# Optimization experiments

Hardware: AMD Instinct MI355X
Metric: run time of the kernel (lower is better)

## Reference

```python
import jax, jax.numpy as jnp
import numpy as np

SEQ, BZ, DIM = 2048, 16, 1024
NUM_LANG, DICT_LEN = 16, 32000


def setup_inputs() -> dict:
    key = jax.random.key(0)
    ks = jax.random.split(key, 6)
    x = jax.random.normal(ks[0], (SEQ, BZ, DIM), dtype=jnp.float32)
    # raw language ids live at the tail of the dictionary: dict_len-1-raw in [0, num_lang)
    raw = DICT_LEN - 1 - jax.random.randint(ks[1], (BZ,), 0, NUM_LANG)
    W_base = jax.random.normal(ks[2], (DIM, DIM), dtype=jnp.float32) * (DIM ** -0.5)
    b_base = jax.random.normal(ks[3], (DIM,), dtype=jnp.float32) * 0.02
    W = jax.random.uniform(ks[4], (NUM_LANG, DIM, DIM), dtype=jnp.float32) * (DIM ** -0.5)
    bias = jax.random.uniform(ks[5], (NUM_LANG, DIM), dtype=jnp.float32)
    return {"x": x, "lang_ids": raw, "W_base": W_base, "b_base": b_base,
            "W": W, "bias": bias, "dict_len": DICT_LEN, "num_lang": NUM_LANG}


def reference(x, lang_ids, W_base, b_base, W, bias, dict_len, num_lang):
    # Map raw ids to expert indices in [0, num_lang)
    ids = dict_len - 1 - lang_ids                      # [bz]
    # base_model (nn.Linear): h = x @ W_base.T + b_base
    h = jnp.einsum('sbd,ed->sbe', x, W_base) + b_base  # [seq, bz, dim]
    # The original pads each language group to max group size, runs a batched
    # einsum 'abcd,ade->abce' over languages, then scatters back with per-lang
    # bias. Mathematically each batch column j gets W[lang_j] applied:
    We = W[ids]                                        # [bz, dim, dim]
    out = jnp.einsum('sbd,bde->sbe', h, We) + bias[ids][None, :, :]
    return out
```

## Files before the change

kernel.cpp:

```cpp
#include <hip/hip_runtime.h>
#include <stdint.h>

typedef unsigned short u16;
typedef unsigned int u32;
typedef __bf16 bf16x8 __attribute__((ext_vector_type(8)));
typedef float f32x4 __attribute__((ext_vector_type(4)));

#define SEQ 2048
#define BZ 16
#define DIM 1024

__device__ __forceinline__ u16 f2bf(float f) {
    union { float f; u32 u; } a; a.f = f;
    u32 r = a.u + 0x7FFFu + ((a.u >> 16) & 1u);
    return (u16)(r >> 16);
}
__device__ __forceinline__ float bf2f(u16 u) {
    union { u32 u; float f; } a; a.u = ((u32)u) << 16;
    return a.f;
}
__device__ __forceinline__ void async16(const u16* g, u16* l) {
    __builtin_amdgcn_global_load_lds(
        (const __attribute__((address_space(1))) void*)g,
        (__attribute__((address_space(3))) void*)l, 16, 0, 0);
}

__global__ void convert_x(const float* __restrict__ x, u16* __restrict__ xb)
{
    int s = blockIdx.x;
    int t = threadIdx.x;
    const float4* src = (const float4*)(x + (size_t)s * BZ * DIM);
    #pragma unroll
    for (int j = 0; j < 16; j++) {
        int idx = j * 256 + t;
        float4 v = src[idx];
        int e = idx * 4;
        int b = e >> 10, d = e & 1023;
        u32 lo = f2bf(v.x) | ((u32)f2bf(v.y) << 16);
        u32 hi = f2bf(v.z) | ((u32)f2bf(v.w) << 16);
        *(uint2*)(xb + ((size_t)b * SEQ + s) * DIM + d) = make_uint2(lo, hi);
    }
}

__global__ void transpose_cvt(const float* __restrict__ W,
                              const float* __restrict__ W_base,
                              const int* __restrict__ lang_ids,
                              const int* __restrict__ dict_len,
                              u16* __restrict__ Wt,
                              u16* __restrict__ Wbt)
{
    int z = blockIdx.z;
    const float* S;
    u16* D;
    if (z < BZ) {
        int id = dict_len[0] - 1 - lang_ids[z];
        S = W + (size_t)id * DIM * DIM;
        D = Wbt + (size_t)z * DIM * DIM;
    } else {
        S = W_base;
        D = Wt;
    }
    __shared__ float tile[32][33];
    int tx = threadIdx.x, ty = threadIdx.y;
    int x0 = blockIdx.x * 32, y0 = blockIdx.y * 32;
    #pragma unroll
    for (int i = 0; i < 4; i++)
        tile[ty + 8 * i][tx] = S[(size_t)(y0 + ty + 8 * i) * DIM + x0 + tx];
    __syncthreads();
    #pragma unroll
    for (int i = 0; i < 4; i++)
        D[(size_t)(x0 + ty + 8 * i) * DIM + y0 + tx] = f2bf(tile[tx][ty + 8 * i]);
}

__global__ void bb_kernel(const u16* __restrict__ Wbt,
                          const float* __restrict__ b_base,
                          const float* __restrict__ bias,
                          const int* __restrict__ lang_ids,
                          const int* __restrict__ dict_len,
                          float* __restrict__ bb)
{
    int gw = blockIdx.x * 4 + (threadIdx.x >> 6);
    int b = gw >> 10;
    int f = gw & 1023;
    int lane = threadIdx.x & 63;
    const u16* row = Wbt + ((size_t)b * DIM + f) * DIM;
    float s = 0.f;
    #pragma unroll
    for (int i = 0; i < DIM / 64; i++)
        s += bf2f(row[lane + 64 * i]) * b_base[lane + 64 * i];
    #pragma unroll
    for (int off = 32; off; off >>= 1)
        s += __shfl_xor(s, off, 64);
    if (lane == 0) {
        int id = dict_len[0] - 1 - lang_ids[b];
        bb[b * DIM + f] = s + bias[(size_t)id * DIM + f];
    }
}

__global__ void gemm1_kernel(const u16* __restrict__ Wbt,
                             const u16* __restrict__ Wt,
                             u16* __restrict__ CT)
{
    int b = blockIdx.z;
    int f0 = blockIdx.y * 128;
    int d0 = blockIdx.x * 128;
    const u16* A = Wbt + (size_t)b * DIM * DIM;
    const u16* B = Wt;
    u16* C = CT + (size_t)b * DIM * DIM;

    __shared__ u16 As[128 * 32];
    __shared__ u16 Bs[128 * 32];

    int tid = threadIdx.x;
    int wave = tid >> 6, lane = tid & 63;
    int wm = (wave >> 1) * 64, wn = (wave & 1) * 64;
    int quad = lane >> 4, lr = lane & 15;

    int srow = wave * 32 + (lane >> 2);
    int scol = (lane & 3) * 8;
    const u16* ga0 = A + (size_t)(f0 + srow) * DIM + scol;
    const u16* ga1 = ga0 + (size_t)16 * DIM;
    const u16* gb0 = B + (size_t)(d0 + srow) * DIM + scol;
    const u16* gb1 = gb0 + (size_t)16 * DIM;
    u16* la0 = &As[(wave * 32) * 32];
    u16* la1 = &As[(wave * 32 + 16) * 32];
    u16* lb0 = &Bs[(wave * 32) * 32];
    u16* lb1 = &Bs[(wave * 32 + 16) * 32];

    f32x4 acc[4][4];
    #pragma unroll
    for (int i = 0; i < 4; i++)
        #pragma unroll
        for (int j = 0; j < 4; j++)
            #pragma unroll
            for (int e = 0; e < 4; e++) acc[i][j][e] = 0.f;

    for (int k0 = 0; k0 < DIM; k0 += 32) {
        async16(ga0, la0); async16(ga1, la1);
        async16(gb0, lb0); async16(gb1, lb1);
        ga0 += 32; ga1 += 32; gb0 += 32; gb1 += 32;
        __syncthreads();
        bf16x8 af[4], bfv[4];
        #pragma unroll
        for (int mt = 0; mt < 4; mt++)
            af[mt] = *(const bf16x8*)&As[(wm + mt * 16 + lr) * 32 + quad * 8];
        #pragma unroll
        for (int nt = 0; nt < 4; nt++)
            bfv[nt] = *(const bf16x8*)&Bs[(wn + nt * 16 + lr) * 32 + quad * 8];
        #pragma unroll
        for (int mt = 0; mt < 4; mt++)
            #pragma unroll
            for (int nt = 0; nt < 4; nt++)
                acc[mt][nt] = __builtin_amdgcn_mfma_f32_16x16x32_bf16(
                    af[mt], bfv[nt], acc[mt][nt], 0, 0, 0);
        __syncthreads();
    }
    #pragma unroll
    for (int mt = 0; mt < 4; mt++) {
        int fr = f0 + wm + mt * 16 + quad * 4;
        #pragma unroll
        for (int nt = 0; nt < 4; nt++) {
            int dc = d0 + wn + nt * 16 + lr;
            #pragma unroll
            for (int rr = 0; rr < 4; rr++)
                C[(size_t)(fr + rr) * DIM + dc] = f2bf(acc[mt][nt][rr]);
        }
    }
}

__global__ void gemm2_kernel(const u16* __restrict__ xb,
                             const u16* __restrict__ CT,
                             const float* __restrict__ bb,
                             float* __restrict__ out)
{
    int b = blockIdx.z;
    int s0 = blockIdx.y * 128;
    int f0 = blockIdx.x * 128;
    const u16* A = xb + (size_t)b * SEQ * DIM;
    const u16* Bm = CT + (size_t)b * DIM * DIM;

    __shared__ u16 As[128 * 32];
    __shared__ u16 Bs[128 * 32];

    int tid = threadIdx.x;
    int wave = tid >> 6, lane = tid & 63;
    int wm = (wave >> 1) * 64, wn = (wave & 1) * 64;
    int quad = lane >> 4, lr = lane & 15;

    int srow = wave * 32 + (lane >> 2);
    int scol = (lane & 3) * 8;
    const u16* ga0 = A + (size_t)(s0 + srow) * DIM + scol;
    const u16* ga1 = ga0 + (size_t)16 * DIM;
    const u16* gb0 = Bm + (size_t)(f0 + srow) * DIM + scol;
    const u16* gb1 = gb0 + (size_t)16 * DIM;
    u16* la0 = &As[(wave * 32) * 32];
    u16* la1 = &As[(wave * 32 + 16) * 32];
    u16* lb0 = &Bs[(wave * 32) * 32];
    u16* lb1 = &Bs[(wave * 32 + 16) * 32];

    f32x4 acc[4][4];
    #pragma unroll
    for (int i = 0; i < 4; i++)
        #pragma unroll
        for (int j = 0; j < 4; j++)
            #pragma unroll
            for (int e = 0; e < 4; e++) acc[i][j][e] = 0.f;

    for (int k0 = 0; k0 < DIM; k0 += 32) {
        async16(ga0, la0); async16(ga1, la1);
        async16(gb0, lb0); async16(gb1, lb1);
        ga0 += 32; ga1 += 32; gb0 += 32; gb1 += 32;
        __syncthreads();
        bf16x8 af[4], bfv[4];
        #pragma unroll
        for (int mt = 0; mt < 4; mt++)
            af[mt] = *(const bf16x8*)&As[(wm + mt * 16 + lr) * 32 + quad * 8];
        #pragma unroll
        for (int nt = 0; nt < 4; nt++)
            bfv[nt] = *(const bf16x8*)&Bs[(wn + nt * 16 + lr) * 32 + quad * 8];
        #pragma unroll
        for (int mt = 0; mt < 4; mt++)
            #pragma unroll
            for (int nt = 0; nt < 4; nt++)
                acc[mt][nt] = __builtin_amdgcn_mfma_f32_16x16x32_bf16(
                    af[mt], bfv[nt], acc[mt][nt], 0, 0, 0);
        __syncthreads();
    }
    #pragma unroll
    for (int nt = 0; nt < 4; nt++) {
        int fcol = f0 + wn + nt * 16 + lr;
        float bv = bb[b * DIM + fcol];
        #pragma unroll
        for (int mt = 0; mt < 4; mt++) {
            int sr = s0 + wm + mt * 16 + quad * 4;
            #pragma unroll
            for (int rr = 0; rr < 4; rr++)
                out[((size_t)(sr + rr) * BZ + b) * DIM + fcol] = acc[mt][nt][rr] + bv;
        }
    }
}

extern "C" void kernel_launch(void* const* d_in, const int* in_sizes, int n_in,
                              void* d_out, int out_size, void* d_ws, size_t ws_size,
                              hipStream_t stream)
{
    const float* x        = (const float*)d_in[0];
    const int*   lang_ids = (const int*)d_in[1];
    const float* W_base   = (const float*)d_in[2];
    const float* b_base   = (const float*)d_in[3];
    const float* W        = (const float*)d_in[4];
    const float* bias     = (const float*)d_in[5];
    const int*   dict_len = (const int*)d_in[6];
    float* out = (float*)d_out;

    char* ws = (char*)d_ws;
    u16*  Wt  = (u16*)ws;
    u16*  Wbt = (u16*)(ws + (size_t)(2u << 20));
    u16*  CT  = (u16*)(ws + (size_t)(34u << 20));
    float* bb = (float*)(ws + (size_t)(66u << 20));
    u16*  xb  = (u16*)(ws + (size_t)(67u << 20));

    convert_x<<<dim3(SEQ, 1, 1), 256, 0, stream>>>(x, xb);
    transpose_cvt<<<dim3(32, 32, 17), dim3(32, 8, 1), 0, stream>>>(
        W, W_base, lang_ids, dict_len, Wt, Wbt);
    bb_kernel<<<dim3(4096, 1, 1), 256, 0, stream>>>(
        Wbt, b_base, bias, lang_ids, dict_len, bb);
    gemm1_kernel<<<dim3(8, 8, 16), 256, 0, stream>>>(Wbt, Wt, CT);
    gemm2_kernel<<<dim3(8, 16, 16), 256, 0, stream>>>(xb, CT, bb, out);
}
```

Measured before the change: 454.9 us.

## Double-buffer LDS tiles and remap GEMM blocks across XCDs

Both GEMM kernels now keep two LDS buffers and issue async global-to-LDS loads for the next K-slice while the current slice feeds MFMA, so load latency overlaps with compute. The 3D grid is flattened to 1D and remapped so that consecutive block IDs, which the hardware spreads round-robin over XCDs, land on the same batch and tile neighbourhood, aiming to improve L2 reuse per XCD. LDS use per block doubles, which may lower occupancy. The loop still relies on the trailing __syncthreads to make the prefetched data visible.

```diff
diff --git a/kernel.cpp b/kernel.cpp
--- a/kernel.cpp
+++ b/kernel.cpp
@@ -101,15 +101,19 @@
                              const u16* __restrict__ Wt,
                              u16* __restrict__ CT)
 {
-    int b = blockIdx.z;
-    int f0 = blockIdx.y * 128;
-    int d0 = blockIdx.x * 128;
+    int bid = blockIdx.x;
+    int virt = ((bid & 7) << 7) + (bid >> 3);
+    int b    = virt >> 6;
+    int rem  = virt & 63;
+    int f0   = (rem >> 3) << 7;
+    int d0   = (rem & 7) << 7;
+
     const u16* A = Wbt + (size_t)b * DIM * DIM;
     const u16* B = Wt;
     u16* C = CT + (size_t)b * DIM * DIM;
 
-    __shared__ u16 As[128 * 32];
-    __shared__ u16 Bs[128 * 32];
+    __shared__ u16 As[2 * 128 * 32];
+    __shared__ u16 Bs[2 * 128 * 32];
 
     int tid = threadIdx.x;
     int wave = tid >> 6, lane = tid & 63;
@@ -122,10 +126,7 @@
     const u16* ga1 = ga0 + (size_t)16 * DIM;
     const u16* gb0 = B + (size_t)(d0 + srow) * DIM + scol;
     const u16* gb1 = gb0 + (size_t)16 * DIM;
-    u16* la0 = &As[(wave * 32) * 32];
-    u16* la1 = &As[(wave * 32 + 16) * 32];
-    u16* lb0 = &Bs[(wave * 32) * 32];
-    u16* lb1 = &Bs[(wave * 32 + 16) * 32];
+    int lofs = wave * 32 * 32;
 
     f32x4 acc[4][4];
     #pragma unroll
@@ -135,18 +136,30 @@
             #pragma unroll
             for (int e = 0; e < 4; e++) acc[i][j][e] = 0.f;
 
+    async16(ga0, As + lofs); async16(ga1, As + lofs + 16 * 32);
+    async16(gb0, Bs + lofs); async16(gb1, Bs + lofs + 16 * 32);
+    ga0 += 32; ga1 += 32; gb0 += 32; gb1 += 32;
+    __syncthreads();
+
+    int cur = 0;
     for (int k0 = 0; k0 < DIM; k0 += 32) {
-        async16(ga0, la0); async16(ga1, la1);
-        async16(gb0, lb0); async16(gb1, lb1);
-        ga0 += 32; ga1 += 32; gb0 += 32; gb1 += 32;
-        __syncthreads();
+        int nxt = cur ^ 1;
+        if (k0 + 32 < DIM) {
+            u16* da = As + nxt * 4096 + lofs;
+            u16* db = Bs + nxt * 4096 + lofs;
+            async16(ga0, da); async16(ga1, da + 16 * 32);
+            async16(gb0, db); async16(gb1, db + 16 * 32);
+            ga0 += 32; ga1 += 32; gb0 += 32; gb1 += 32;
+        }
+        const u16* ra = As + cur * 4096;
+        const u16* rb = Bs + cur * 4096;
         bf16x8 af[4], bfv[4];
         #pragma unroll
         for (int mt = 0; mt < 4; mt++)
-            af[mt] = *(const bf16x8*)&As[(wm + mt * 16 + lr) * 32 + quad * 8];
+            af[mt] = *(const bf16x8*)&ra[(wm + mt * 16 + lr) * 32 + quad * 8];
         #pragma unroll
         for (int nt = 0; nt < 4; nt++)
-            bfv[nt] = *(const bf16x8*)&Bs[(wn + nt * 16 + lr) * 32 + quad * 8];
+            bfv[nt] = *(const bf16x8*)&rb[(wn + nt * 16 + lr) * 32 + quad * 8];
         #pragma unroll
         for (int mt = 0; mt < 4; mt++)
             #pragma unroll
@@ -154,6 +167,7 @@
                 acc[mt][nt] = __builtin_amdgcn_mfma_f32_16x16x32_bf16(
                     af[mt], bfv[nt], acc[mt][nt], 0, 0, 0);
         __syncthreads();
+        cur = nxt;
     }
     #pragma unroll
     for (int mt = 0; mt < 4; mt++) {
@@ -173,14 +187,18 @@
                              const float* __restrict__ bb,
                              float* __restrict__ out)
 {
-    int b = blockIdx.z;
-    int s0 = blockIdx.y * 128;
-    int f0 = blockIdx.x * 128;
-    const u16* A = xb + (size_t)b * SEQ * DIM;
+    int bid = blockIdx.x;
+    int virt = ((bid & 7) << 8) + (bid >> 3);
+    int b    = virt >> 7;
+    int rem  = virt & 127;
+    int s0   = (rem >> 3) << 7;
+    int f0   = (rem & 7) << 7;
+
+    const u16* A  = xb + (size_t)b * SEQ * DIM;
     const u16* Bm = CT + (size_t)b * DIM * DIM;
 
-    __shared__ u16 As[128 * 32];
-    __shared__ u16 Bs[128 * 32];
+    __shared__ u16 As[2 * 128 * 32];
+    __shared__ u16 Bs[2 * 128 * 32];
 
     int tid = threadIdx.x;
     int wave = tid >> 6, lane = tid & 63;
@@ -193,10 +211,7 @@
     const u16* ga1 = ga0 + (size_t)16 * DIM;
     const u16* gb0 = Bm + (size_t)(f0 + srow) * DIM + scol;
     const u16* gb1 = gb0 + (size_t)16 * DIM;
-    u16* la0 = &As[(wave * 32) * 32];
-    u16* la1 = &As[(wave * 32 + 16) * 32];
-    u16* lb0 = &Bs[(wave * 32) * 32];
-    u16* lb1 = &Bs[(wave * 32 + 16) * 32];
+    int lofs = wave * 32 * 32;
 
     f32x4 acc[4][4];
     #pragma unroll
@@ -206,18 +221,30 @@
             #pragma unroll
             for (int e = 0; e < 4; e++) acc[i][j][e] = 0.f;
 
+    async16(ga0, As + lofs); async16(ga1, As + lofs + 16 * 32);
+    async16(gb0, Bs + lofs); async16(gb1, Bs + lofs + 16 * 32);
+    ga0 += 32; ga1 += 32; gb0 += 32; gb1 += 32;
+    __syncthreads();
+
+    int cur = 0;
     for (int k0 = 0; k0 < DIM; k0 += 32) {
-        async16(ga0, la0); async16(ga1, la1);
-        async16(gb0, lb0); async16(gb1, lb1);
-        ga0 += 32; ga1 += 32; gb0 += 32; gb1 += 32;
-        __syncthreads();
+        int nxt = cur ^ 1;
+        if (k0 + 32 < DIM) {
+            u16* da = As + nxt * 4096 + lofs;
+            u16* db = Bs + nxt * 4096 + lofs;
+            async16(ga0, da); async16(ga1, da + 16 * 32);
+            async16(gb0, db); async16(gb1, db + 16 * 32);
+            ga0 += 32; ga1 += 32; gb0 += 32; gb1 += 32;
+        }
+        const u16* ra = As + cur * 4096;
+        const u16* rb = Bs + cur * 4096;
         bf16x8 af[4], bfv[4];
         #pragma unroll
         for (int mt = 0; mt < 4; mt++)
-            af[mt] = *(const bf16x8*)&As[(wm + mt * 16 + lr) * 32 + quad * 8];
+            af[mt] = *(const bf16x8*)&ra[(wm + mt * 16 + lr) * 32 + quad * 8];
         #pragma unroll
         for (int nt = 0; nt < 4; nt++)
-            bfv[nt] = *(const bf16x8*)&Bs[(wn + nt * 16 + lr) * 32 + quad * 8];
+            bfv[nt] = *(const bf16x8*)&rb[(wn + nt * 16 + lr) * 32 + quad * 8];
         #pragma unroll
         for (int mt = 0; mt < 4; mt++)
             #pragma unroll
@@ -225,6 +252,7 @@
                 acc[mt][nt] = __builtin_amdgcn_mfma_f32_16x16x32_bf16(
                     af[mt], bfv[nt], acc[mt][nt], 0, 0, 0);
         __syncthreads();
+        cur = nxt;
     }
     #pragma unroll
     for (int nt = 0; nt < 4; nt++) {
@@ -265,6 +293,6 @@
         W, W_base, lang_ids, dict_len, Wt, Wbt);
     bb_kernel<<<dim3(4096, 1, 1), 256, 0, stream>>>(
         Wbt, b_base, bias, lang_ids, dict_len, bb);
-    gemm1_kernel<<<dim3(8, 8, 16), 256, 0, stream>>>(Wbt, Wt, CT);
-    gemm2_kernel<<<dim3(8, 16, 16), 256, 0, stream>>>(xb, CT, bb, out);
-}
+    gemm1_kernel<<<dim3(1024, 1, 1), 256, 0, stream>>>(Wbt, Wt, CT);
+    gemm2_kernel<<<dim3(2048, 1, 1), 256, 0, stream>>>(xb, CT, bb, out);
+}
```

Measured after the change: 425.6 us. -6.4%, faster.
